# Performance work log

Measured on AMD Instinct MI355X. Metric: run time of the kernel, lower is better.

## Reference

```python
import jax, jax.numpy as jnp
import numpy as np
from jax import lax

# (class_index, min, max) triples: 13 combinations x 3 conditions
_COMBOS = np.array([
    [(500, 0.1, 0.8), (41, 0.05, 0.5), (0, 0.0, 1.0)],
    [(369, 0.1, 0.5), (500, 0.1, 0.5), (0, 0.0, 1.0)],
    [(412, 0.05, 0.4), (431, 0.05, 0.4), (470, 0.05, 0.4)],
    [(127, 0.1, 0.8), (67, 0.1, 0.7), (103, 0.1, 0.6)],
    [(399, 0.1, 0.9), (403, 0.1, 0.8), (412, 0.1, 0.7)],
    [(410, 0.1, 0.9), (411, 0.1, 0.8), (398, 0.1, 0.7)],
    [(412, 0.1, 0.8), (410, 0.1, 0.7), (398, 0.1, 0.6)],
    [(435, 0.1, 0.9), (438, 0.1, 0.8), (449, 0.1, 0.7)],
    [(374, 0.1, 0.9), (436, 0.1, 0.8), (435, 0.1, 0.7)],
    [(372, 0.1, 0.9), (434, 0.1, 0.8), (469, 0.1, 0.7)],
    [(500, 0.1, 0.8), (439, 0.1, 0.7), (50, 0.1, 0.6)],
    [(399, 0.1, 0.9), (403, 0.1, 0.8), (410, 0.1, 0.7)],
    [(410, 0.1, 0.9), (398, 0.1, 0.8), (435, 0.1, 0.7)],
], dtype=np.float32)  # (13, 3, 3)
_CLASS_IDX = jnp.asarray(_COMBOS[:, :, 0].astype(np.int32))  # (13, 3)
_MINS = jnp.asarray(_COMBOS[:, :, 1])  # (13, 3)
_MAXS = jnp.asarray(_COMBOS[:, :, 2])  # (13, 3)
_BRUX_SCORE = jnp.asarray(np.array([2.94, 1.76, 1.76, 1.47, 0.29, 0.88, 0.01, 0.29, 0.29, 0.01, 0.29, 0.01, 0.01], dtype=np.float32))
_NON_BRUX = jnp.asarray(np.array([38, 42, 0], dtype=np.int32))


def setup_inputs() -> dict:
    key = jax.random.key(0)
    score = jax.random.uniform(key, (1, 512), dtype=jnp.float32)
    return {"score": score}


def reference(score):
    s = jnp.squeeze(score, axis=0)  # (C,)
    # Vectorized equivalent of the sequential while_loop with early exit:
    # per-combination pass flag (all 3 conditions in range)
    vals = s[_CLASS_IDX]  # (13, 3)
    in_range = (vals >= _MINS) & (vals <= _MAXS)
    combo_pass = jnp.all(in_range, axis=1)  # (13,)
    any_pass = jnp.any(combo_pass)
    first_idx = jnp.argmax(combo_pass)  # index of first passing combo (== index-1 in TF loop)
    # top-10 must NOT contain any non-bruxism class
    _, top10 = lax.top_k(s, 10)
    has_non_brux = jnp.any(top10[:, None] == _NON_BRUX[None, :])
    judgement = any_pass & jnp.logical_not(has_non_brux)
    value = jnp.where(judgement, jnp.round(_BRUX_SCORE[first_idx] * 100.0) / 100.0, jnp.float32(0.0))
    return judgement, value
```

## Files before the change

### kernel.cpp

```cpp
#include <hip/hip_runtime.h>
#include <hip/hip_bf16.h>


#define N_COMBOS 13

__global__ __launch_bounds__(64)
void bruxism_judge_kernel(const float* __restrict__ score, float* __restrict__ out) {
    __shared__ float s_lds[512];

    const int t = threadIdx.x;

    const float4 a = reinterpret_cast<const float4*>(score)[t];
    const float4 b = reinterpret_cast<const float4*>(score)[64 + t];

    reinterpret_cast<float4*>(s_lds)[t]      = a;
    reinterpret_cast<float4*>(s_lds)[64 + t] = b;

    const float v[8]  = {a.x, a.y, a.z, a.w, b.x, b.y, b.z, b.w};

    const float s38 = __shfl(a.z, 9);
    const float s42 = __shfl(a.z, 10);
    const float s0  = __shfl(a.x, 0);

    int packed = 0;
    #pragma unroll
    for (int e = 0; e < 8; ++e) {
        const float x = v[e];
        const int   j = (e < 4) ? (4 * t + e) : (256 + 4 * t + (e - 4));
        packed += ((x > s38) || ((x == s38) && (j < 38))) ? (1 << 0)  : 0;
        packed += ((x > s42) || ((x == s42) && (j < 42))) ? (1 << 10) : 0;
        packed += ( (x > s0)                            ) ? (1 << 20) : 0;
    }
    #pragma unroll
    for (int off = 32; off >= 1; off >>= 1) packed += __shfl_xor(packed, off);

    const int cnt38 = (packed >> 0)  & 1023;
    const int cnt42 = (packed >> 10) & 1023;
    const int cnt0  = (packed >> 20) & 1023;
    const bool has_non_brux = (cnt38 < 10) || (cnt42 < 10) || (cnt0 < 10);

    constexpr int cls[N_COMBOS][3] = {
        {500,  41,   0}, {369, 500,   0}, {412, 431, 470}, {127,  67, 103},
        {399, 403, 412}, {410, 411, 398}, {412, 410, 398}, {435, 438, 449},
        {374, 436, 435}, {372, 434, 469}, {500, 439,  50}, {399, 403, 410},
        {410, 398, 435},
    };
    constexpr float cmin[N_COMBOS][3] = {
        {0.10f, 0.05f, 0.00f}, {0.10f, 0.10f, 0.00f}, {0.05f, 0.05f, 0.05f},
        {0.10f, 0.10f, 0.10f}, {0.10f, 0.10f, 0.10f}, {0.10f, 0.10f, 0.10f},
        {0.10f, 0.10f, 0.10f}, {0.10f, 0.10f, 0.10f}, {0.10f, 0.10f, 0.10f},
        {0.10f, 0.10f, 0.10f}, {0.10f, 0.10f, 0.10f}, {0.10f, 0.10f, 0.10f},
        {0.10f, 0.10f, 0.10f},
    };
    constexpr float cmax[N_COMBOS][3] = {
        {0.8f, 0.5f, 1.0f}, {0.5f, 0.5f, 1.0f}, {0.4f, 0.4f, 0.4f},
        {0.8f, 0.7f, 0.6f}, {0.9f, 0.8f, 0.7f}, {0.9f, 0.8f, 0.7f},
        {0.8f, 0.7f, 0.6f}, {0.9f, 0.8f, 0.7f}, {0.9f, 0.8f, 0.7f},
        {0.9f, 0.8f, 0.7f}, {0.8f, 0.7f, 0.6f}, {0.9f, 0.8f, 0.7f},
        {0.9f, 0.8f, 0.7f},
    };
    constexpr float brux[N_COMBOS] = {
        2.94f, 1.76f, 1.76f, 1.47f, 0.29f, 0.88f, 0.01f,
        0.29f, 0.29f, 0.01f, 0.29f, 0.01f, 0.01f
    };

    bool any_pass = false;
    int  first    = 0;
    #pragma unroll
    for (int i = N_COMBOS - 1; i >= 0; --i) {
        bool pass = true;
        #pragma unroll
        for (int j = 0; j < 3; ++j) {
            const float val = s_lds[cls[i][j]];
            pass = pass && (val >= cmin[i][j]) && (val <= cmax[i][j]);
        }
        if (pass) { any_pass = true; first = i; }
    }

    if (t == 0) {
        const bool judgement = any_pass && !has_non_brux;
        float bs = brux[0];
        #pragma unroll
        for (int i = 1; i < N_COMBOS; ++i) bs = (first == i) ? brux[i] : bs;
        const float value = judgement ? (rintf(bs * 100.0f) / 100.0f) : 0.0f;
        float2 o = make_float2(judgement ? 1.0f : 0.0f, value);
        *reinterpret_cast<float2*>(out) = o;
    }
}

extern "C" void kernel_launch(void* const* d_in, const int* in_sizes, int n_in,
                              void* d_out, int out_size, void* d_ws, size_t ws_size,
                              hipStream_t stream) {
    const float* score = (const float*)d_in[0];
    float* out = (float*)d_out;
    bruxism_judge_kernel<<<1, 64, 0, stream>>>(score, out);
}
```

Measured before the change: 9.737 us.

## Replace shuffle reduction and LDS staging with ballot counts and direct global loads

Drops the shared-memory staging of the score vector and reads the combo class values and pivot scores directly from global memory (cached scalar/vector loads). The packed shfl_xor butterfly reduction is replaced by per-condition ballot+popcount counts, and the rounding of the bruxism score is folded into precomputed constants. This aims to remove LDS writes/reads and the shuffle reduction latency in a single-wave kernel, at the cost of more global loads that should hit cache.

Measured after the change: 10.14 us. +4.1%, slower.

```diff
diff --git a/kernel.cpp b/kernel.cpp
--- a/kernel.cpp
+++ b/kernel.cpp
@@ -6,37 +6,25 @@
 
 __global__ __launch_bounds__(64)
 void bruxism_judge_kernel(const float* __restrict__ score, float* __restrict__ out) {
-    __shared__ float s_lds[512];
-
     const int t = threadIdx.x;
 
     const float4 a = reinterpret_cast<const float4*>(score)[t];
     const float4 b = reinterpret_cast<const float4*>(score)[64 + t];
+    const float v[8] = {a.x, a.y, a.z, a.w, b.x, b.y, b.z, b.w};
 
-    reinterpret_cast<float4*>(s_lds)[t]      = a;
-    reinterpret_cast<float4*>(s_lds)[64 + t] = b;
+    const float s38 = score[38];
+    const float s42 = score[42];
+    const float s0  = score[0];
 
-    const float v[8]  = {a.x, a.y, a.z, a.w, b.x, b.y, b.z, b.w};
-
-    const float s38 = __shfl(a.z, 9);
-    const float s42 = __shfl(a.z, 10);
-    const float s0  = __shfl(a.x, 0);
-
-    int packed = 0;
+    int cnt38 = 0, cnt42 = 0, cnt0 = 0;
     #pragma unroll
     for (int e = 0; e < 8; ++e) {
         const float x = v[e];
         const int   j = (e < 4) ? (4 * t + e) : (256 + 4 * t + (e - 4));
-        packed += ((x > s38) || ((x == s38) && (j < 38))) ? (1 << 0)  : 0;
-        packed += ((x > s42) || ((x == s42) && (j < 42))) ? (1 << 10) : 0;
-        packed += ( (x > s0)                            ) ? (1 << 20) : 0;
+        cnt38 += __popcll(__ballot((x > s38) || ((x == s38) && (j < 38))));
+        cnt42 += __popcll(__ballot((x > s42) || ((x == s42) && (j < 42))));
+        cnt0  += __popcll(__ballot( x > s0 ));
     }
-    #pragma unroll
-    for (int off = 32; off >= 1; off >>= 1) packed += __shfl_xor(packed, off);
-
-    const int cnt38 = (packed >> 0)  & 1023;
-    const int cnt42 = (packed >> 10) & 1023;
-    const int cnt0  = (packed >> 20) & 1023;
     const bool has_non_brux = (cnt38 < 10) || (cnt42 < 10) || (cnt0 < 10);
 
     constexpr int cls[N_COMBOS][3] = {
@@ -59,31 +47,30 @@
         {0.9f, 0.8f, 0.7f}, {0.8f, 0.7f, 0.6f}, {0.9f, 0.8f, 0.7f},
         {0.9f, 0.8f, 0.7f},
     };
-    constexpr float brux[N_COMBOS] = {
-        2.94f, 1.76f, 1.76f, 1.47f, 0.29f, 0.88f, 0.01f,
-        0.29f, 0.29f, 0.01f, 0.29f, 0.01f, 0.01f
+    constexpr float bval[N_COMBOS] = {
+        294.0f / 100.0f, 176.0f / 100.0f, 176.0f / 100.0f, 147.0f / 100.0f,
+         29.0f / 100.0f,  88.0f / 100.0f,   1.0f / 100.0f,  29.0f / 100.0f,
+         29.0f / 100.0f,   1.0f / 100.0f,  29.0f / 100.0f,   1.0f / 100.0f,
+          1.0f / 100.0f,
     };
 
-    bool any_pass = false;
-    int  first    = 0;
+    bool  any_pass = false;
+    float value_if = bval[0];
     #pragma unroll
     for (int i = N_COMBOS - 1; i >= 0; --i) {
         bool pass = true;
         #pragma unroll
         for (int j = 0; j < 3; ++j) {
-            const float val = s_lds[cls[i][j]];
+            const float val = score[cls[i][j]];
             pass = pass && (val >= cmin[i][j]) && (val <= cmax[i][j]);
         }
-        if (pass) { any_pass = true; first = i; }
+        if (pass) { any_pass = true; value_if = bval[i]; }
     }
 
     if (t == 0) {
         const bool judgement = any_pass && !has_non_brux;
-        float bs = brux[0];
-        #pragma unroll
-        for (int i = 1; i < N_COMBOS; ++i) bs = (first == i) ? brux[i] : bs;
-        const float value = judgement ? (rintf(bs * 100.0f) / 100.0f) : 0.0f;
-        float2 o = make_float2(judgement ? 1.0f : 0.0f, value);
+        float2 o = make_float2(judgement ? 1.0f : 0.0f,
+                               judgement ? value_if : 0.0f);
         *reinterpret_cast<float2*>(out) = o;
     }
 }
```
